# Optimization experiments

Hardware: AMD Instinct MI355X
Metric: run time of the kernel (lower is better)

Reference implementation:

```python
import jax, jax.numpy as jnp
import numpy as np


def setup_inputs() -> dict:
    key = jax.random.key(0)
    ks = jax.random.split(key, 5)
    B, S, D, U = 4, 2048, 1024, 1024
    scale = 1.0 / np.sqrt(D)
    return {
        "query": jax.random.normal(ks[0], (B, S, D), dtype=jnp.float32),
        "value": jax.random.normal(ks[1], (B, S, D), dtype=jnp.float32),
        "Wq": jax.random.normal(ks[2], (D, U), dtype=jnp.float32) * scale,
        "bq": jnp.zeros((U,), dtype=jnp.float32),
        "Wk": jax.random.normal(ks[3], (D, U), dtype=jnp.float32) * scale,
        "bk": jnp.zeros((U,), dtype=jnp.float32),
        "Wv": jax.random.normal(ks[4], (D, U), dtype=jnp.float32) * scale,
        "bv": jnp.zeros((U,), dtype=jnp.float32),
    }


def reference(query, value, Wq, bq, Wk, bk, Wv, bv):
    # Dense projections (last-dim matmul + bias)
    Q = jnp.einsum("bsd,du->bsu", query, Wq) + bq   # [B,Sq,U]
    K = jnp.einsum("btd,du->btu", value, Wk) + bk   # [B,Sk,U]
    V = jnp.einsum("btd,du->btu", value, Wv) + bv   # [B,Sk,U]
    d_k = jnp.asarray(K.shape[-1], dtype=jnp.float32)
    scores = jnp.einsum("bsu,btu->bst", Q, K) / jnp.sqrt(d_k)  # [B,Sq,Sk]
    weights = jax.nn.softmax(scores, axis=-1)
    return jnp.einsum("bst,btu->bsu", weights, V)   # [B,Sq,U]
```

## Files before the change

### kernel.cpp

```cpp
#include <hip/hip_runtime.h>
#include <hip/hip_bf16.h>
#include <stdint.h>

#define DEVINL __device__ __forceinline__

typedef __attribute__((ext_vector_type(4))) float f32x4;
typedef __attribute__((ext_vector_type(8))) __bf16 bfv8;
typedef __attribute__((ext_vector_type(8))) short s16x8;
typedef __attribute__((ext_vector_type(4))) short s16x4;

DEVINL short f2bf(float f) {
  union { float f; unsigned u; } v; v.f = f;
  unsigned r = v.u + 0x7FFFu + ((v.u >> 16) & 1u);
  return (short)(r >> 16);
}
DEVINL float bf2f(short h) {
  union { unsigned u; float f; } v; v.u = ((unsigned)(unsigned short)h) << 16;
  return v.f;
}
DEVINL void gload_lds16(const void* g, void* l) {
  __builtin_amdgcn_global_load_lds((__attribute__((address_space(1))) unsigned*)(g),
                                   (__attribute__((address_space(3))) unsigned*)(l),
                                   16, 0, 0);
}
#define S_BARRIER() __builtin_amdgcn_s_barrier()
#define MEMORD() asm volatile("" ::: "memory")
template <int N> DEVINL void vmwaitc() {
  asm volatile("s_waitcnt vmcnt(%0)" :: "i"(N) : "memory");
}
DEVINL int xswz(int p, int n) { return (p & 7) * (n >> 3) + (p >> 3); }

DEVINL void gemm64_core(const short* __restrict__ Ag, const short* __restrict__ Bg,
                        int lda, int ldb, int m0, int n0, int nkt,
                        short* lds, f32x4 (&acc)[8][4]) {
  const int tid = threadIdx.x;
  const int w = tid >> 6, l = tid & 63;
  const int wm = w >> 2, wn = w & 3;
  const int lr = l & 15, lg = l >> 4;
  const int srow = 8 * w + (l >> 3);
  const int scol = (((l & 7) ^ ((l >> 3) & 7)) << 3);
  const int dW = w * 512;
  const int xk0 = ((lg ^ (lr & 7)) << 3);
  const int xk1 = (((4 + lg) ^ (lr & 7)) << 3);
  const int aoff = (wm * 128 + lr) * 64;
  const int boff = 16384 + (wn * 64 + lr) * 64;

#define SG_A(t, h) { short* S_ = lds + (((t) & 1) ? 32768 : 0) + (h) * 8192;              \
    gload_lds16(Ag + (size_t)(m0 + 128 * (h) + srow) * lda + (t) * 64 + scol, S_ + dW);   \
    gload_lds16(Ag + (size_t)(m0 + 128 * (h) + 64 + srow) * lda + (t) * 64 + scol,        \
                S_ + 4096 + dW); }
#define SG_B(t, h) { short* S_ = lds + (((t) & 1) ? 32768 : 0) + 16384 + (h) * 8192;      \
    gload_lds16(Bg + (size_t)(n0 + 128 * (h) + srow) * ldb + (t) * 64 + scol, S_ + dW);   \
    gload_lds16(Bg + (size_t)(n0 + 128 * (h) + 64 + srow) * ldb + (t) * 64 + scol,        \
                S_ + 4096 + dW); }
#define MFMA_QUAD(M0, M1)                                                                 \
    _Pragma("unroll")                                                                     \
    for (int nf = 0; nf < 4; ++nf) {                                                      \
      acc[M0][nf] = __builtin_amdgcn_mfma_f32_16x16x32_bf16(a00, br[nf][0], acc[M0][nf], 0, 0, 0); \
      acc[M0][nf] = __builtin_amdgcn_mfma_f32_16x16x32_bf16(a01, br[nf][1], acc[M0][nf], 0, 0, 0); \
      acc[M1][nf] = __builtin_amdgcn_mfma_f32_16x16x32_bf16(a10, br[nf][0], acc[M1][nf], 0, 0, 0); \
      acc[M1][nf] = __builtin_amdgcn_mfma_f32_16x16x32_bf16(a11, br[nf][1], acc[M1][nf], 0, 0, 0); \
    }

  SG_A(0, 0); SG_A(0, 1); SG_B(0, 0); SG_B(0, 1);
  vmwaitc<0>(); S_BARRIER(); MEMORD();

#pragma unroll 1
  for (int kt = 0; kt < nkt; ++kt) {
    const short* S = lds + ((kt & 1) ? 32768 : 0);
    const bool pf = (kt + 1 < nkt);
    bfv8 br[4][2];
#pragma unroll
    for (int nf = 0; nf < 4; ++nf) {
      br[nf][0] = *(const bfv8*)(S + boff + nf * 1024 + xk0);
      br[nf][1] = *(const bfv8*)(S + boff + nf * 1024 + xk1);
    }
    bfv8 a00 = *(const bfv8*)(S + aoff + 0 * 1024 + xk0);
    bfv8 a01 = *(const bfv8*)(S + aoff + 0 * 1024 + xk1);
    bfv8 a10 = *(const bfv8*)(S + aoff + 1 * 1024 + xk0);
    bfv8 a11 = *(const bfv8*)(S + aoff + 1 * 1024 + xk1);
    if (pf) { SG_A(kt + 1, 0); SG_A(kt + 1, 1); }
    S_BARRIER();
    __builtin_amdgcn_s_setprio(1);
    MFMA_QUAD(0, 1);
    __builtin_amdgcn_s_setprio(0);
    S_BARRIER(); MEMORD();
    a00 = *(const bfv8*)(S + aoff + 2 * 1024 + xk0);
    a01 = *(const bfv8*)(S + aoff + 2 * 1024 + xk1);
    a10 = *(const bfv8*)(S + aoff + 3 * 1024 + xk0);
    a11 = *(const bfv8*)(S + aoff + 3 * 1024 + xk1);
    if (pf) SG_B(kt + 1, 0);
    S_BARRIER();
    __builtin_amdgcn_s_setprio(1);
    MFMA_QUAD(2, 3);
    __builtin_amdgcn_s_setprio(0);
    S_BARRIER(); MEMORD();
    a00 = *(const bfv8*)(S + aoff + 4 * 1024 + xk0);
    a01 = *(const bfv8*)(S + aoff + 4 * 1024 + xk1);
    a10 = *(const bfv8*)(S + aoff + 5 * 1024 + xk0);
    a11 = *(const bfv8*)(S + aoff + 5 * 1024 + xk1);
    if (pf) SG_B(kt + 1, 1);
    S_BARRIER();
    __builtin_amdgcn_s_setprio(1);
    MFMA_QUAD(4, 5);
    __builtin_amdgcn_s_setprio(0);
    S_BARRIER(); MEMORD();
    a00 = *(const bfv8*)(S + aoff + 6 * 1024 + xk0);
    a01 = *(const bfv8*)(S + aoff + 6 * 1024 + xk1);
    a10 = *(const bfv8*)(S + aoff + 7 * 1024 + xk0);
    a11 = *(const bfv8*)(S + aoff + 7 * 1024 + xk1);
    if (pf) vmwaitc<0>();
    S_BARRIER();
    __builtin_amdgcn_s_setprio(1);
    MFMA_QUAD(6, 7);
    __builtin_amdgcn_s_setprio(0);
    S_BARRIER(); MEMORD();
  }
#undef SG_A
#undef SG_B
#undef MFMA_QUAD
}

template <int BU, int NF, int RING>
DEVINL void gemm_core(const short* __restrict__ Ag, const short* __restrict__ Bg,
                      int lda, int ldb, int m0, int n0, int nkt,
                      short* lds, f32x4 (&acc)[8][NF]) {
  constexpr int U = 2 + BU;
  constexpr int SLOT = 8192 + BU * 4096;
  const int tid = threadIdx.x;
  const int w = tid >> 6, l = tid & 63;
  const int wm = w >> 2, wn = w & 3;
  const int lr = l & 15, lg = l >> 4;
  const int stg_row = w * 16 + (l >> 2);
  const int stg_col = (((l & 3) ^ ((l >> 3) & 3)) << 3);
  const int ck = ((lg ^ ((lr >> 1) & 3)) << 3);
  const int aro = (wm * 128 + lr) * 32 + ck;
  const int bro = 8192 + (wn * (NF * 16) + lr) * 32 + ck;
  const int dW = w * 512;
#define STAGE_A(t) { short* S_ = lds + ((t) % RING) * SLOT;                                \
    gload_lds16(Ag + (size_t)(m0 + stg_row) * lda + (t) * 32 + stg_col, S_ + dW);          \
    gload_lds16(Ag + (size_t)(m0 + 128 + stg_row) * lda + (t) * 32 + stg_col,              \
                S_ + 4096 + dW); }
#define STAGE_B(t) { short* S_ = lds + ((t) % RING) * SLOT;                                \
    _Pragma("unroll")                                                                      \
    for (int u_ = 0; u_ < BU; ++u_)                                                        \
      gload_lds16(Bg + (size_t)(n0 + u_ * 128 + stg_row) * ldb + (t) * 32 + stg_col,       \
                  S_ + 8192 + u_ * 4096 + dW); }
#pragma unroll
  for (int t = 0; t < RING - 1; ++t) { STAGE_A(t); STAGE_B(t); }
  vmwaitc<(RING - 2) * U>(); S_BARRIER(); MEMORD();
  bfv8 aA[4], aB[4], bA[NF], bB[NF];
  {
    const short* Sp = lds;
#pragma unroll
    for (int mf = 0; mf < 4; ++mf) aA[mf] = *(const bfv8*)(Sp + aro + mf * 512);
#pragma unroll
    for (int nf = 0; nf < NF; ++nf) bA[nf] = *(const bfv8*)(Sp + bro + nf * 512);
  }
#pragma unroll 1
  for (int kt = 0; kt < nkt; kt += 2) {
    const short* S1 = lds + ((kt + 1) % RING) * SLOT;
    const short* S2 = lds + ((kt + 2) % RING) * SLOT;
    const short* S0 = lds + (kt % RING) * SLOT;
    if (kt + 2 < nkt) STAGE_A(kt + 2);
#pragma unroll
    for (int mf = 0; mf < 4; ++mf) aB[mf] = *(const bfv8*)(S0 + aro + 2048 + mf * 512);
#pragma unroll
    for (int mf = 0; mf < 4; ++mf)
#pragma unroll
      for (int nf = 0; nf < NF; ++nf)
        acc[mf][nf] = __builtin_amdgcn_mfma_f32_16x16x32_bf16(aA[mf], bA[nf], acc[mf][nf], 0, 0, 0);
    if (kt + 2 < nkt) vmwaitc<2>(); else vmwaitc<0>();
    S_BARRIER(); MEMORD();
    if (kt + 2 < nkt) STAGE_B(kt + 2);
#pragma unroll
    for (int mf = 0; mf < 4; ++mf) aA[mf] = *(const bfv8*)(S1 + aro + mf * 512);
#pragma unroll
    for (int nf = 0; nf < NF; ++nf) bB[nf] = *(const bfv8*)(S1 + bro + nf * 512);
#pragma unroll
    for (int mf = 0; mf < 4; ++mf)
#pragma unroll
      for (int nf = 0; nf < NF; ++nf)
        acc[4 + mf][nf] = __builtin_amdgcn_mfma_f32_16x16x32_bf16(aB[mf], bA[nf], acc[4 + mf][nf], 0, 0, 0);
    S_BARRIER(); MEMORD();
    if (kt + 3 < nkt) STAGE_A(kt + 3);
#pragma unroll
    for (int mf = 0; mf < 4; ++mf) aB[mf] = *(const bfv8*)(S1 + aro + 2048 + mf * 512);
#pragma unroll
    for (int mf = 0; mf < 4; ++mf)
#pragma unroll
      for (int nf = 0; nf < NF; ++nf)
        acc[mf][nf] = __builtin_amdgcn_mfma_f32_16x16x32_bf16(aA[mf], bB[nf], acc[mf][nf], 0, 0, 0);
    if (kt + 3 < nkt) vmwaitc<2>(); else vmwaitc<0>();
    S_BARRIER(); MEMORD();
    if (kt + 3 < nkt) STAGE_B(kt + 3);
    if (kt + 2 < nkt) {
#pragma unroll
      for (int mf = 0; mf < 4; ++mf) aA[mf] = *(const bfv8*)(S2 + aro + mf * 512);
#pragma unroll
      for (int nf = 0; nf < NF; ++nf) bA[nf] = *(const bfv8*)(S2 + bro + nf * 512);
    }
#pragma unroll
    for (int mf = 0; mf < 4; ++mf)
#pragma unroll
      for (int nf = 0; nf < NF; ++nf)
        acc[4 + mf][nf] = __builtin_amdgcn_mfma_f32_16x16x32_bf16(aB[mf], bB[nf], acc[4 + mf][nf], 0, 0, 0);
    S_BARRIER(); MEMORD();
  }
#undef STAGE_A
#undef STAGE_B
}

__global__ __launch_bounds__(256) void prep_kernel(
    const float* __restrict__ q, const float* __restrict__ v,
    const float* __restrict__ Wq, const float* __restrict__ Wk, const float* __restrict__ Wv,
    short* __restrict__ Qc, short* __restrict__ Vc,
    short* __restrict__ WTq, short* __restrict__ WTk, short* __restrict__ WTv) {
  __shared__ float tile[64][65];
  const int bx = blockIdx.x;
  if (bx < 8192) {
    const float* src = (bx < 4096) ? q : v;
    short* dst = (bx < 4096) ? Qc : Vc;
    const size_t i = ((size_t)(bx & 4095) * 256 + threadIdx.x) * 8;
    f32x4 x0 = *(const f32x4*)(src + i);
    f32x4 x1 = *(const f32x4*)(src + i + 4);
    s16x8 o;
#pragma unroll
    for (int j = 0; j < 4; ++j) { o[j] = f2bf(x0[j]); o[4 + j] = f2bf(x1[j]); }
    *(s16x8*)(dst + i) = o;
  } else {
    const int z = (bx - 8192) >> 8, xx = (bx - 8192) & 255;
    const float* W = (z == 0) ? Wq : (z == 1) ? Wk : Wv;
    short* WT = (z == 0) ? WTq : (z == 1) ? WTk : WTv;
    const int k0 = (xx & 15) << 6, n0 = (xx >> 4) << 6;
    const int c = threadIdx.x & 63, r0 = threadIdx.x >> 6;
#pragma unroll
    for (int i = 0; i < 16; ++i) {
      int r = (i << 2) + r0;
      tile[r][c] = W[(size_t)(k0 + r) * 1024 + n0 + c];
    }
    __syncthreads();
#pragma unroll
    for (int i = 0; i < 16; ++i) {
      int a = (i << 2) + r0;
      WT[(size_t)(n0 + a) * 1024 + k0 + c] = f2bf(tile[c][a]);
    }
  }
}

__global__ __launch_bounds__(512, 2) void qkproj_kernel(
    const short* __restrict__ Qc, const short* __restrict__ Vc,
    const short* __restrict__ WTq, const short* __restrict__ WTk,
    const float* __restrict__ bq, const float* __restrict__ bk,
    short* __restrict__ Qb, short* __restrict__ Kb) {
  __shared__ short lds[65536];
  const int o = xswz(blockIdx.x, 256);
  const int sel = o >> 7, r = o & 127;
  const int bm = r >> 2, bn = r & 3;
  const short* A = sel ? Vc : Qc;
  const short* BT = sel ? WTk : WTq;
  const float* bias = sel ? bk : bq;
  short* O = sel ? Kb : Qb;
  const int m0 = bm * 256, n0 = bn * 256;
  f32x4 acc[8][4];
#pragma unroll
  for (int i = 0; i < 8; ++i)
#pragma unroll
    for (int j = 0; j < 4; ++j) acc[i][j] = (f32x4){0.f, 0.f, 0.f, 0.f};
  gemm64_core(A, BT, 1024, 1024, m0, n0, 16, lds, acc);
  const int tid = threadIdx.x;
  const int w = tid >> 6, l = tid & 63;
  const int wm = w >> 2, wn = w & 3, lr = l & 15, lg = l >> 4;
#pragma unroll
  for (int mf = 0; mf < 8; ++mf) {
    const int row0 = m0 + wm * 128 + mf * 16 + lg * 4;
#pragma unroll
    for (int nf = 0; nf < 4; ++nf) {
      const int col = n0 + wn * 64 + nf * 16 + lr;
      const float bb = bias[col];
#pragma unroll
      for (int j = 0; j < 4; ++j)
        O[(size_t)(row0 + j) * 1024 + col] = f2bf(acc[mf][nf][j] + bb);
    }
  }
}

__global__ __launch_bounds__(512, 2) void vproj_kernel(
    const short* __restrict__ Vc, const short* __restrict__ WTv,
    const float* __restrict__ bv, short* __restrict__ VT) {
  __shared__ short lds[36864];
  const int o = xswz(blockIdx.x, 256);
  const int bm = o >> 3, bn = o & 7;
  const int m0 = bm * 256, n0 = bn * 128;
  f32x4 acc[8][2];
#pragma unroll
  for (int i = 0; i < 8; ++i)
#pragma unroll
    for (int j = 0; j < 2; ++j) acc[i][j] = (f32x4){0.f, 0.f, 0.f, 0.f};
  gemm_core<1, 2, 3>(Vc, WTv, 1024, 1024, m0, n0, 32, lds, acc);
  const int tid = threadIdx.x;
  const int w = tid >> 6, l = tid & 63;
  const int wm = w >> 2, wn = w & 3, lr = l & 15, lg = l >> 4;
  __syncthreads();
  short* lt = lds;
#pragma unroll
  for (int i = 0; i < 8; ++i) {
    const int tl = wm * 128 + (i >> 2) * 64 + (i & 3) * 16 + lg * 4;
#pragma unroll
    for (int nf = 0; nf < 2; ++nf) {
      const int ul = wn * 32 + nf * 16 + lr;
      const float bb = bv[n0 + ul];
      s16x4 pk;
#pragma unroll
      for (int j = 0; j < 4; ++j) pk[j] = f2bf(acc[i][nf][j] + bb);
      *(s16x4*)&lt[ul * 264 + tl] = pk;
    }
  }
  __syncthreads();
  const int b = m0 >> 11, t0 = m0 & 2047;
#pragma unroll
  for (int it = 0; it < 8; ++it) {
    const int cid = it * 512 + tid;
    const int u = cid >> 5, tc = cid & 31;
    s16x8 v8 = *(const s16x8*)&lt[u * 264 + tc * 8];
    *(s16x8*)(VT + ((size_t)b * 1024 + n0 + u) * 2048 + t0 + tc * 8) = v8;
  }
}

__global__ __launch_bounds__(512, 2) void qkt_kernel(const short* __restrict__ Qb,
                                                     const short* __restrict__ Kb,
                                                     short* __restrict__ Sb) {
  __shared__ short lds[65536];
  const int o = xswz(blockIdx.x, 256);
  const int bt = o >> 6, r = o & 63;
  const int bm = r >> 3, bn = r & 7;
  const short* A = Qb + (size_t)bt * 2097152;
  const short* B = Kb + (size_t)bt * 2097152;
  short* O = Sb + (size_t)bt * 4194304;
  const int m0 = bm * 256, n0 = bn * 256;
  f32x4 acc[8][4];
#pragma unroll
  for (int i = 0; i < 8; ++i)
#pragma unroll
    for (int j = 0; j < 4; ++j) acc[i][j] = (f32x4){0.f, 0.f, 0.f, 0.f};
  gemm64_core(A, B, 1024, 1024, m0, n0, 16, lds, acc);
  const int tid = threadIdx.x;
  const int w = tid >> 6, l = tid & 63;
  const int wm = w >> 2, wn = w & 3, lr = l & 15, lg = l >> 4;
#pragma unroll
  for (int mf = 0; mf < 8; ++mf) {
    const int row0 = m0 + wm * 128 + mf * 16 + lg * 4;
#pragma unroll
    for (int nf = 0; nf < 4; ++nf) {
      const int col = n0 + wn * 64 + nf * 16 + lr;
#pragma unroll
      for (int j = 0; j < 4; ++j)
        O[(size_t)(row0 + j) * 2048 + col] = f2bf(acc[mf][nf][j] * 0.03125f);
    }
  }
}

__global__ __launch_bounds__(512, 2) void pv_kernel(const short* __restrict__ Sb,
                                                    const short* __restrict__ VT,
                                                    float* __restrict__ Out,
                                                    float* __restrict__ Part) {
  __shared__ short lds[65536];
  const int o = xswz(blockIdx.x, 256);
  const int kh = o >> 7;
  const int bt = (o >> 5) & 3;
  const int bm = (o >> 2) & 7, bn = o & 3;
  const short* A = Sb + (size_t)bt * 4194304 + kh * 1024;
  const short* B = VT + (size_t)bt * 2097152 + kh * 1024;
  float* O = (kh ? Part : Out) + (size_t)bt * 2097152;
  const int m0 = bm * 256, n0 = bn * 256;
  f32x4 acc[8][4];
#pragma unroll
  for (int i = 0; i < 8; ++i)
#pragma unroll
    for (int j = 0; j < 4; ++j) acc[i][j] = (f32x4){0.f, 0.f, 0.f, 0.f};
  gemm64_core(A, B, 2048, 2048, m0, n0, 16, lds, acc);
  const int l = threadIdx.x & 63, w = threadIdx.x >> 6;
  const int wm = w >> 2, wn = w & 3, lr = l & 15, lg = l >> 4;
#pragma unroll
  for (int mf = 0; mf < 8; ++mf) {
    const int row0 = m0 + wm * 128 + mf * 16 + lg * 4;
#pragma unroll
    for (int nf = 0; nf < 4; ++nf) {
      const int col = n0 + wn * 64 + nf * 16 + lr;
#pragma unroll
      for (int j = 0; j < 4; ++j)
        O[(size_t)(row0 + j) * 1024 + col] = acc[mf][nf][j];
    }
  }
}

__global__ __launch_bounds__(256) void add_kernel(float* __restrict__ Out,
                                                  const float* __restrict__ Part) {
  const size_t i = ((size_t)blockIdx.x * 256 + threadIdx.x) * 4;
  f32x4 a = *(const f32x4*)(Out + i);
  f32x4 b = *(const f32x4*)(Part + i);
#pragma unroll
  for (int j = 0; j < 4; ++j) a[j] += b[j];
  *(f32x4*)(Out + i) = a;
}

__global__ __launch_bounds__(256) void softmax_kernel(short* __restrict__ Sb) {
  const size_t row = blockIdx.x;
  short* p = Sb + row * 2048;
  const int tid = threadIdx.x;
  const int w = tid >> 6, l = tid & 63;
  s16x8 v = *(const s16x8*)(p + tid * 8);
  float f[8];
#pragma unroll
  for (int j = 0; j < 8; ++j) f[j] = bf2f(v[j]);
  float m = f[0];
#pragma unroll
  for (int j = 1; j < 8; ++j) m = fmaxf(m, f[j]);
#pragma unroll
  for (int o = 32; o > 0; o >>= 1) m = fmaxf(m, __shfl_xor(m, o, 64));
  __shared__ float redm[4], reds[4];
  if (l == 0) redm[w] = m;
  __syncthreads();
  m = fmaxf(fmaxf(redm[0], redm[1]), fmaxf(redm[2], redm[3]));
  float s = 0.f;
#pragma unroll
  for (int j = 0; j < 8; ++j) { f[j] = __expf(f[j] - m); s += f[j]; }
#pragma unroll
  for (int o = 32; o > 0; o >>= 1) s += __shfl_xor(s, o, 64);
  if (l == 0) reds[w] = s;
  __syncthreads();
  s = reds[0] + reds[1] + reds[2] + reds[3];
  const float inv = 1.f / s;
  s16x8 o8;
#pragma unroll
  for (int j = 0; j < 8; ++j) o8[j] = f2bf(f[j] * inv);
  *(s16x8*)(p + tid * 8) = o8;
}

extern "C" void kernel_launch(void* const* d_in, const int* in_sizes, int n_in,
                              void* d_out, int out_size, void* d_ws, size_t ws_size,
                              hipStream_t stream) {
  const float* query = (const float*)d_in[0];
  const float* value = (const float*)d_in[1];
  const float* Wq = (const float*)d_in[2];
  const float* bq = (const float*)d_in[3];
  const float* Wk = (const float*)d_in[4];
  const float* bk = (const float*)d_in[5];
  const float* Wv = (const float*)d_in[6];
  const float* bv = (const float*)d_in[7];

  char* ws = (char*)d_ws;
  short* WTq = (short*)(ws);
  short* WTk = (short*)(ws + ((size_t)2 << 20));
  short* WTv = (short*)(ws + ((size_t)4 << 20));
  short* Qc  = (short*)(ws + ((size_t)6 << 20));
  short* Vc  = (short*)(ws + ((size_t)22 << 20));
  short* Sb  = (short*)(ws + ((size_t)6 << 20));
  short* Qb  = (short*)(ws + ((size_t)38 << 20));
  short* Kb  = (short*)(ws + ((size_t)54 << 20));
  float* Part = (float*)(ws + ((size_t)38 << 20));
  short* VT  = (short*)(ws + ((size_t)70 << 20));

  prep_kernel<<<dim3(8960), 256, 0, stream>>>(query, value, Wq, Wk, Wv, Qc, Vc, WTq, WTk, WTv);

  qkproj_kernel<<<dim3(256), 512, 0, stream>>>(Qc, Vc, WTq, WTk, bq, bk, Qb, Kb);
  vproj_kernel<<<dim3(256), 512, 0, stream>>>(Vc, WTv, bv, VT);

  qkt_kernel<<<dim3(256), 512, 0, stream>>>(Qb, Kb, Sb);

  softmax_kernel<<<dim3(8192), 256, 0, stream>>>(Sb);

  pv_kernel<<<dim3(256), 512, 0, stream>>>(Sb, VT, (float*)d_out, Part);
  add_kernel<<<dim3(8192), 256, 0, stream>>>((float*)d_out, Part);
}
```

Baseline: 190.5 us.

## Use a three-slot A ring with two-deep prefetch and a single B buffer

After: 190.5 us. No clear change (-0.0%).

```diff
diff --git a/kernel.cpp b/kernel.cpp
--- a/kernel.cpp
+++ b/kernel.cpp
@@ -43,16 +43,18 @@
   const int xk0 = ((lg ^ (lr & 7)) << 3);
   const int xk1 = (((4 + lg) ^ (lr & 7)) << 3);
   const int aoff = (wm * 128 + lr) * 64;
-  const int boff = 16384 + (wn * 64 + lr) * 64;
-
-#define SG_A(t, h) { short* S_ = lds + (((t) & 1) ? 32768 : 0) + (h) * 8192;              \
-    gload_lds16(Ag + (size_t)(m0 + 128 * (h) + srow) * lda + (t) * 64 + scol, S_ + dW);   \
-    gload_lds16(Ag + (size_t)(m0 + 128 * (h) + 64 + srow) * lda + (t) * 64 + scol,        \
-                S_ + 4096 + dW); }
-#define SG_B(t, h) { short* S_ = lds + (((t) & 1) ? 32768 : 0) + 16384 + (h) * 8192;      \
-    gload_lds16(Bg + (size_t)(n0 + 128 * (h) + srow) * ldb + (t) * 64 + scol, S_ + dW);   \
-    gload_lds16(Bg + (size_t)(n0 + 128 * (h) + 64 + srow) * ldb + (t) * 64 + scol,        \
-                S_ + 4096 + dW); }
+  const int boff = 49152 + (wn * 64 + lr) * 64;
+
+#define SG_A4(t, ring) { short* S_ = lds + (ring) * 16384;                                \
+    _Pragma("unroll")                                                                     \
+    for (int q_ = 0; q_ < 4; ++q_)                                                        \
+      gload_lds16(Ag + (size_t)(m0 + 64 * q_ + srow) * lda + (t) * 64 + scol,             \
+                  S_ + q_ * 4096 + dW); }
+#define SG_B4(t) { short* S_ = lds + 49152;                                               \
+    _Pragma("unroll")                                                                     \
+    for (int q_ = 0; q_ < 4; ++q_)                                                        \
+      gload_lds16(Bg + (size_t)(n0 + 64 * q_ + srow) * ldb + (t) * 64 + scol,             \
+                  S_ + q_ * 4096 + dW); }
 #define MFMA_QUAD(M0, M1)                                                                 \
     _Pragma("unroll")                                                                     \
     for (int nf = 0; nf < 4; ++nf) {                                                      \
@@ -62,24 +64,25 @@
       acc[M1][nf] = __builtin_amdgcn_mfma_f32_16x16x32_bf16(a11, br[nf][1], acc[M1][nf], 0, 0, 0); \
     }
 
-  SG_A(0, 0); SG_A(0, 1); SG_B(0, 0); SG_B(0, 1);
-  vmwaitc<0>(); S_BARRIER(); MEMORD();
-
+  SG_A4(0, 0); SG_B4(0);
+  if (nkt > 1) SG_A4(1, 1);
+  if (nkt > 1) vmwaitc<4>(); else vmwaitc<0>();
+  S_BARRIER(); MEMORD();
+
+  int ra = 0;
 #pragma unroll 1
   for (int kt = 0; kt < nkt; ++kt) {
-    const short* S = lds + ((kt & 1) ? 32768 : 0);
-    const bool pf = (kt + 1 < nkt);
+    const short* S = lds + ra * 16384;
     bfv8 br[4][2];
 #pragma unroll
     for (int nf = 0; nf < 4; ++nf) {
-      br[nf][0] = *(const bfv8*)(S + boff + nf * 1024 + xk0);
-      br[nf][1] = *(const bfv8*)(S + boff + nf * 1024 + xk1);
+      br[nf][0] = *(const bfv8*)(lds + boff + nf * 1024 + xk0);
+      br[nf][1] = *(const bfv8*)(lds + boff + nf * 1024 + xk1);
     }
     bfv8 a00 = *(const bfv8*)(S + aoff + 0 * 1024 + xk0);
     bfv8 a01 = *(const bfv8*)(S + aoff + 0 * 1024 + xk1);
     bfv8 a10 = *(const bfv8*)(S + aoff + 1 * 1024 + xk0);
     bfv8 a11 = *(const bfv8*)(S + aoff + 1 * 1024 + xk1);
-    if (pf) { SG_A(kt + 1, 0); SG_A(kt + 1, 1); }
     S_BARRIER();
     __builtin_amdgcn_s_setprio(1);
     MFMA_QUAD(0, 1);
@@ -89,7 +92,7 @@
     a01 = *(const bfv8*)(S + aoff + 2 * 1024 + xk1);
     a10 = *(const bfv8*)(S + aoff + 3 * 1024 + xk0);
     a11 = *(const bfv8*)(S + aoff + 3 * 1024 + xk1);
-    if (pf) SG_B(kt + 1, 0);
+    if (kt + 1 < nkt) SG_B4(kt + 1);
     S_BARRIER();
     __builtin_amdgcn_s_setprio(1);
     MFMA_QUAD(2, 3);
@@ -99,7 +102,10 @@
     a01 = *(const bfv8*)(S + aoff + 4 * 1024 + xk1);
     a10 = *(const bfv8*)(S + aoff + 5 * 1024 + xk0);
     a11 = *(const bfv8*)(S + aoff + 5 * 1024 + xk1);
-    if (pf) SG_B(kt + 1, 1);
+    if (kt + 2 < nkt) {
+      int r2 = ra + 2; if (r2 >= 3) r2 -= 3;
+      SG_A4(kt + 2, r2);
+    }
     S_BARRIER();
     __builtin_amdgcn_s_setprio(1);
     MFMA_QUAD(4, 5);
@@ -109,15 +115,17 @@
     a01 = *(const bfv8*)(S + aoff + 6 * 1024 + xk1);
     a10 = *(const bfv8*)(S + aoff + 7 * 1024 + xk0);
     a11 = *(const bfv8*)(S + aoff + 7 * 1024 + xk1);
-    if (pf) vmwaitc<0>();
     S_BARRIER();
     __builtin_amdgcn_s_setprio(1);
     MFMA_QUAD(6, 7);
     __builtin_amdgcn_s_setprio(0);
-    S_BARRIER(); MEMORD();
-  }
-#undef SG_A
-#undef SG_B
+    if (kt + 2 < nkt) vmwaitc<4>();
+    else if (kt + 1 < nkt) vmwaitc<0>();
+    S_BARRIER(); MEMORD();
+    ra = (ra + 1 == 3) ? 0 : ra + 1;
+  }
+#undef SG_A4
+#undef SG_B4
 #undef MFMA_QUAD
 }
 
```
